# Kernel tuning notes

Hardware: AMD Instinct MI355X
Metric: run time of the kernel (lower is better)

## Reference

```python
import jax, jax.numpy as jnp
import numpy as np

B, L, D, H = 8, 4096, 512, 512  # batch, seq_len, input channels, hidden_dim
EPS = 1e-5


def setup_inputs() -> dict:
    key = jax.random.key(0)
    ks = jax.random.split(key, 6)
    sD = 1.0 / np.sqrt(D)
    sH = 1.0 / np.sqrt(H)
    return {
        "x": jax.random.normal(ks[0], (B, L, D), jnp.float32),
        "ln_gamma": jnp.ones((D,), jnp.float32),
        "ln_beta": jnp.zeros((D,), jnp.float32),
        "W_B": jax.random.normal(ks[1], (D, H), jnp.float32) * sD,
        "b_B": jnp.zeros((H,), jnp.float32),
        "W_C": jax.random.normal(ks[2], (D, H), jnp.float32) * sD,
        "b_C": jnp.zeros((H,), jnp.float32),
        "W_out": jax.random.normal(ks[3], (H, H), jnp.float32) * sH,
        "b_out": jnp.zeros((H,), jnp.float32),
        # original initializes A to zeros; use decays in (0,1) for a non-trivial scan
        "A": jax.random.uniform(ks[4], (H,), jnp.float32, 0.1, 0.95),
    }


def _scan_op(e1, e2):
    # composition of affine maps h -> a*h + b (elementwise, per channel)
    a1, b1 = e1
    a2, b2 = e2
    return a1 * a2, a2 * b1 + b2


def reference(x, ln_gamma, ln_beta, W_B, b_B, W_C, b_C, W_out, b_out, A):
    # LayerNorm over channels
    mu = jnp.mean(x, axis=-1, keepdims=True)
    var = jnp.var(x, axis=-1, keepdims=True)
    xn = (x - mu) * jax.lax.rsqrt(var + EPS) * ln_gamma + ln_beta  # [B,L,D]

    Bt = jnp.einsum("bld,dh->blh", xn, W_B) + b_B  # [B,L,H]
    Ct = jnp.einsum("bld,dh->blh", xn, W_C) + b_C  # [B,L,H]

    # linear recurrence h_t = A * h_{t-1} + B_t via associative scan over L
    a_full = jnp.broadcast_to(A, Bt.shape)
    _, h = jax.lax.associative_scan(_scan_op, (a_full, Bt), axis=1)  # [B,L,H]

    y = Ct * h  # selective readout
    return jnp.einsum("blh,ho->blo", y, W_out) + b_out  # [B,L,H]
```

## Files before the change

kernel.cpp:

```cpp
#include <hip/hip_runtime.h>
#include <hip/hip_bf16.h>
#include <stdint.h>

typedef __bf16 bf16x8 __attribute__((ext_vector_type(8)));
typedef float f32x4 __attribute__((ext_vector_type(4)));

constexpr int Bn = 8, Ln = 4096, Dn = 512, Hn = 512;
constexpr int Mrows = Bn * Ln;
constexpr int CHUNK = 64, NCHUNK = Ln / CHUNK;

__global__ __launch_bounds__(256) void prep_kernel(
    const float* __restrict__ W_B, const float* __restrict__ W_C,
    const float* __restrict__ W_out, const float* __restrict__ b_B,
    const float* __restrict__ b_C,
    __hip_bfloat16* __restrict__ WbcT, __hip_bfloat16* __restrict__ WoT,
    float* __restrict__ bbc)
{
    int id = blockIdx.x * 256 + threadIdx.x;
    {
        int n = id >> 9, k = id & 511;
        float w = (n < Hn) ? W_B[k * Hn + n] : W_C[k * Hn + (n - Hn)];
        WbcT[id] = __float2bfloat16(w);
    }
    if (id < Hn * Hn) {
        int n = id >> 9, k = id & 511;
        WoT[id] = __float2bfloat16(W_out[k * Hn + n]);
    }
    if (id < 2 * Hn) bbc[id] = (id < Hn) ? b_B[id] : b_C[id - Hn];
}

__global__ __launch_bounds__(256) void ln_kernel(
    const float* __restrict__ x, const float* __restrict__ gamma,
    const float* __restrict__ beta, __hip_bfloat16* __restrict__ xn)
{
    int row = blockIdx.x;
    const float2* xr = reinterpret_cast<const float2*>(x + (size_t)row * Dn);
    int t = threadIdx.x;
    float2 v = xr[t];
    float s = v.x + v.y;
    float s2 = v.x * v.x + v.y * v.y;
    #pragma unroll
    for (int off = 32; off; off >>= 1) {
        s  += __shfl_down(s, off);
        s2 += __shfl_down(s2, off);
    }
    __shared__ float ps[4], ps2[4];
    int wid = t >> 6, lane = t & 63;
    if (lane == 0) { ps[wid] = s; ps2[wid] = s2; }
    __syncthreads();
    float su = ps[0] + ps[1] + ps[2] + ps[3];
    float su2 = ps2[0] + ps2[1] + ps2[2] + ps2[3];
    float mu = su * (1.0f / Dn);
    float var = su2 * (1.0f / Dn) - mu * mu;
    float inv = rsqrtf(var + 1e-5f);
    int c0 = 2 * t;
    float y0 = (v.x - mu) * inv * gamma[c0]     + beta[c0];
    float y1 = (v.y - mu) * inv * gamma[c0 + 1] + beta[c0 + 1];
    __hip_bfloat162 o;
    o.x = __float2bfloat16(y0);
    o.y = __float2bfloat16(y1);
    reinterpret_cast<__hip_bfloat162*>(xn + (size_t)row * Dn)[t] = o;
}

template <int NT, bool OUT_BF16>
__global__ __launch_bounds__(512, 2) void gemm8_kernel(
    const __hip_bfloat16* __restrict__ A,
    const __hip_bfloat16* __restrict__ BT,
    const float* __restrict__ bias,
    void* __restrict__ Cout)
{
    constexpr int K = 512, NKT = K / 64, NIT = NKT / 2;
    extern __shared__ unsigned short lds[];

    int nwg = gridDim.x, bid = blockIdx.x;
    int bswz = (bid & 7) * (nwg >> 3) + (bid >> 3);
    constexpr int NBN = NT / 256;
    int bm = bswz / NBN, bnb = bswz % NBN;
    int row0 = bm * 256, col0 = bnb * 256;

    int tid = threadIdx.x;
    int w = tid >> 6, l = tid & 63;
    int rl = l & 15, qg = l >> 4, sx = l & 7, r8 = l >> 3;

    int scol = (sx ^ r8) * 8;
    const __hip_bfloat16* gA = A  + (size_t)(row0 + w * 16 + r8) * K + scol;
    const __hip_bfloat16* gB = BT + (size_t)(col0 + w * 16 + r8) * K + scol;

#define LDSA(b, h) (&lds[(b) * 32768 + (h) * 8192 + w * 1024])
#define LDSB(b, h) (&lds[(b) * 32768 + 16384 + (h) * 8192 + w * 1024])
#define GLDS(src, dst) __builtin_amdgcn_global_load_lds( \
        (const __attribute__((address_space(1))) void*)(const void*)(src), \
        (__attribute__((address_space(3))) void*)(void*)(dst), 16, 0, 0)
#define STAGE_A(b, kt, h) { \
        GLDS(gA + (size_t)((h) * 128) * K + (kt) * 64, LDSA(b, h)); \
        GLDS(gA + (size_t)((h) * 128 + 8) * K + (kt) * 64, LDSA(b, h) + 512); }
#define STAGE_B(b, kt, h) { \
        GLDS(gB + (size_t)((h) * 128) * K + (kt) * 64, LDSB(b, h)); \
        GLDS(gB + (size_t)((h) * 128 + 8) * K + (kt) * 64, LDSB(b, h) + 512); }
#define BARRIER { asm volatile("" ::: "memory"); __builtin_amdgcn_s_barrier(); \
                  asm volatile("" ::: "memory"); }
#define VMCNT(n) asm volatile("s_waitcnt vmcnt(" #n ")" ::: "memory")

    int aoff = (w >> 2) * 8192 + rl * 64;
    int boff = 16384 + ((w & 3) >> 1) * 8192 + (((w & 3) & 1) * 64 + rl) * 64;
    int s0 = (qg ^ sx) * 8;

    f32x4 acc[8][4] = {};
    bf16x8 af[4][2], bfr[4][2];

#define RD_A(mq, b) { _Pragma("unroll") for (int i2 = 0; i2 < 4; ++i2) { \
        af[i2][0] = *(const bf16x8*)&lds[(b) * 32768 + aoff + ((mq) * 4 + i2) * 1024 + s0]; \
        af[i2][1] = *(const bf16x8*)&lds[(b) * 32768 + aoff + ((mq) * 4 + i2) * 1024 + (s0 ^ 32)]; } }
#define RD_B(nh, b) { _Pragma("unroll") for (int j2 = 0; j2 < 2; ++j2) { \
        bfr[(nh) * 2 + j2][0] = *(const bf16x8*)&lds[(b) * 32768 + boff + ((nh) * 2 + j2) * 1024 + s0]; \
        bfr[(nh) * 2 + j2][1] = *(const bf16x8*)&lds[(b) * 32768 + boff + ((nh) * 2 + j2) * 1024 + (s0 ^ 32)]; } }
#define MM(mq, nq) { __builtin_amdgcn_s_setprio(1); \
        _Pragma("unroll") for (int i2 = 0; i2 < 4; ++i2) \
        _Pragma("unroll") for (int n2 = 0; n2 < 2; ++n2) \
        _Pragma("unroll") for (int kk = 0; kk < 2; ++kk) \
            acc[(mq) * 4 + i2][(nq) * 2 + n2] = __builtin_amdgcn_mfma_f32_16x16x32_bf16( \
                af[i2][kk], bfr[(nq) * 2 + n2][kk], acc[(mq) * 4 + i2][(nq) * 2 + n2], 0, 0, 0); \
        __builtin_amdgcn_s_setprio(0); }

    STAGE_B(0, 0, 0); STAGE_B(0, 0, 1); STAGE_A(0, 0, 0); STAGE_A(0, 0, 1);
    STAGE_B(1, 1, 0); STAGE_B(1, 1, 1); STAGE_A(1, 1, 0);
    VMCNT(6);
    BARRIER;

    for (int it = 0; it < NIT; ++it) {
        int ktB = 2 * it + 1, ktN = 2 * it + 2;
        bool more = (it < NIT - 1);
        RD_A(0, 0); RD_B(0, 0);
        STAGE_A(1, ktB, 1);
        BARRIER; MM(0, 0); BARRIER;
        RD_B(1, 0);
        if (more) STAGE_B(0, ktN, 0);
        BARRIER; MM(0, 1); BARRIER;
        RD_A(1, 0);
        if (more) STAGE_B(0, ktN, 1);
        BARRIER; MM(1, 1); BARRIER;
        if (more) STAGE_A(0, ktN, 0);
        BARRIER; MM(1, 0);
        if (more) { VMCNT(6); } else { VMCNT(0); }
        BARRIER;
        RD_A(0, 1); RD_B(0, 1);
        if (more) STAGE_A(0, ktN, 1);
        BARRIER; MM(0, 0); BARRIER;
        RD_B(1, 1);
        if (more) STAGE_B(1, ktN + 1, 0);
        BARRIER; MM(0, 1); BARRIER;
        RD_A(1, 1);
        if (more) STAGE_B(1, ktN + 1, 1);
        BARRIER; MM(1, 1); BARRIER;
        if (more) {
            STAGE_A(1, ktN + 1, 0);
            BARRIER; MM(1, 0); VMCNT(6); BARRIER;
        } else {
            MM(1, 0);
        }
    }

    int crow0 = row0 + (w >> 2) * 128 + qg * 4;
    int ccol0 = col0 + (w & 3) * 64 + rl;
    #pragma unroll
    for (int n = 0; n < 4; ++n) {
        float bv = bias[ccol0 + n * 16];
        #pragma unroll
        for (int i = 0; i < 8; ++i) {
            #pragma unroll
            for (int j = 0; j < 4; ++j) {
                float v = acc[i][n][j] + bv;
                size_t idx = (size_t)(crow0 + i * 16 + j) * NT + (ccol0 + n * 16);
                if (OUT_BF16)
                    ((__hip_bfloat16*)Cout)[idx] = __float2bfloat16(v);
                else
                    ((float*)Cout)[idx] = v;
            }
        }
    }
#undef LDSA
#undef LDSB
#undef GLDS
#undef STAGE_A
#undef STAGE_B
#undef BARRIER
#undef VMCNT
#undef RD_A
#undef RD_B
#undef MM
}

__global__ __launch_bounds__(256) void scan1_kernel(
    const __hip_bfloat16* __restrict__ BC, const float* __restrict__ Av,
    float* __restrict__ S)
{
    int blk = blockIdx.x;
    int hh = (blk & 1) * 256 + threadIdx.x;
    int c = (blk >> 1) & (NCHUNK - 1);
    int b = blk >> 7;
    float a = Av[hh];
    const __hip_bfloat16* p = BC + ((size_t)(b * Ln + c * CHUNK) * 1024) + hh;
    float s = 0.f;
    #pragma unroll 8
    for (int i = 0; i < CHUNK; ++i) {
        float bv = __bfloat162float(p[(size_t)i * 1024]);
        s = a * s + bv;
    }
    S[((size_t)b * NCHUNK + c) * Hn + hh] = s;
}

__global__ __launch_bounds__(256) void scan2_kernel(
    const float* __restrict__ S, const float* __restrict__ Av,
    float* __restrict__ carry)
{
    int id = blockIdx.x * 256 + threadIdx.x;
    int hh = id & (Hn - 1), b = id >> 9;
    float a = Av[hh];
    float aG = a;
    #pragma unroll
    for (int i = 0; i < 6; ++i) aG *= aG;
    float h = 0.f;
    const float* Sp = S + (size_t)b * NCHUNK * Hn + hh;
    float* cp = carry + (size_t)b * NCHUNK * Hn + hh;
    for (int c = 0; c < NCHUNK; ++c) {
        cp[(size_t)c * Hn] = h;
        h = aG * h + Sp[(size_t)c * Hn];
    }
}

__global__ __launch_bounds__(256) void scan3_kernel(
    const __hip_bfloat16* __restrict__ BC, const float* __restrict__ Av,
    const float* __restrict__ carry, __hip_bfloat16* __restrict__ Y)
{
    int blk = blockIdx.x;
    int hh = (blk & 1) * 256 + threadIdx.x;
    int c = (blk >> 1) & (NCHUNK - 1);
    int b = blk >> 7;
    float a = Av[hh];
    float h = carry[((size_t)b * NCHUNK + c) * Hn + hh];
    const __hip_bfloat16* p = BC + ((size_t)(b * Ln + c * CHUNK) * 1024) + hh;
    __hip_bfloat16* yp = Y + ((size_t)(b * Ln + c * CHUNK) * Hn) + hh;
    #pragma unroll 8
    for (int i = 0; i < CHUNK; ++i) {
        float bv = __bfloat162float(p[(size_t)i * 1024]);
        float cv = __bfloat162float(p[(size_t)i * 1024 + 512]);
        h = a * h + bv;
        yp[(size_t)i * Hn] = __float2bfloat16(cv * h);
    }
}

extern "C" void kernel_launch(void* const* d_in, const int* in_sizes, int n_in,
                              void* d_out, int out_size, void* d_ws, size_t ws_size,
                              hipStream_t stream)
{
    const float* x     = (const float*)d_in[0];
    const float* ln_g  = (const float*)d_in[1];
    const float* ln_b  = (const float*)d_in[2];
    const float* W_B   = (const float*)d_in[3];
    const float* b_B   = (const float*)d_in[4];
    const float* W_C   = (const float*)d_in[5];
    const float* b_C   = (const float*)d_in[6];
    const float* W_out = (const float*)d_in[7];
    const float* b_out = (const float*)d_in[8];
    const float* Avec  = (const float*)d_in[9];

    char* ws = (char*)d_ws;
    __hip_bfloat16* WbcT = (__hip_bfloat16*)(ws);
    __hip_bfloat16* WoT  = (__hip_bfloat16*)(ws + (1u << 20));
    float*          bbc  = (float*)(ws + (1u << 20) + (1u << 19));
    __hip_bfloat16* XN   = (__hip_bfloat16*)(ws + (2u << 20));
    __hip_bfloat16* BC   = (__hip_bfloat16*)(ws + (34u << 20));
    float*          Sbuf = (float*)(ws + (98u << 20));
    float*          Cbuf = (float*)(ws + (99u << 20));
    __hip_bfloat16* Y    = (__hip_bfloat16*)(ws + (100u << 20));

    hipFuncSetAttribute((const void*)gemm8_kernel<1024, true>,
                        hipFuncAttributeMaxDynamicSharedMemorySize, 131072);
    hipFuncSetAttribute((const void*)gemm8_kernel<512, false>,
                        hipFuncAttributeMaxDynamicSharedMemorySize, 131072);

    prep_kernel<<<2048, 256, 0, stream>>>(W_B, W_C, W_out, b_B, b_C, WbcT, WoT, bbc);
    ln_kernel<<<Mrows, 256, 0, stream>>>(x, ln_g, ln_b, XN);
    gemm8_kernel<1024, true><<<(Mrows / 256) * (1024 / 256), 512, 131072, stream>>>(
        XN, WbcT, bbc, BC);
    scan1_kernel<<<Bn * NCHUNK * 2, 256, 0, stream>>>(BC, Avec, Sbuf);
    scan2_kernel<<<(Bn * Hn) / 256, 256, 0, stream>>>(Sbuf, Avec, Cbuf);
    scan3_kernel<<<Bn * NCHUNK * 2, 256, 0, stream>>>(BC, Avec, Cbuf, Y);
    gemm8_kernel<512, false><<<(Mrows / 256) * (512 / 256), 512, 131072, stream>>>(
        Y, WoT, b_out, d_out);
}
```

Before: 134.5 us.

## Shrink GEMM tiles to 128x128 with 4-wave workgroups

Replaces the 256x256-tile, 8-wave GEMM with a 128x128-tile, 4-wave version that uses 64KB of LDS. The staging schedule, LDS swizzle addressing and wave-to-subtile mapping are rewritten to fit the smaller tile. The aim is more workgroups for better CU load balance and occupancy, since the second GEMM previously launched only 256 blocks. The trade-off is lower data reuse per tile, which means more global/L2 traffic and more LDS reads per MFMA.

After: 136.6 us. No clear change (+1.5%).

```diff
diff --git a/kernel.cpp b/kernel.cpp
--- a/kernel.cpp
+++ b/kernel.cpp
@@ -63,110 +63,109 @@
 }
 
 template <int NT, bool OUT_BF16>
-__global__ __launch_bounds__(512, 2) void gemm8_kernel(
+__global__ __launch_bounds__(256, 2) void gemm4_kernel(
     const __hip_bfloat16* __restrict__ A,
     const __hip_bfloat16* __restrict__ BT,
     const float* __restrict__ bias,
     void* __restrict__ Cout)
 {
-    constexpr int K = 512, NKT = K / 64, NIT = NKT / 2;
+    constexpr int K = 512, NIT = 4;
     extern __shared__ unsigned short lds[];
 
     int nwg = gridDim.x, bid = blockIdx.x;
     int bswz = (bid & 7) * (nwg >> 3) + (bid >> 3);
-    constexpr int NBN = NT / 256;
+    constexpr int NBN = NT / 128;
     int bm = bswz / NBN, bnb = bswz % NBN;
-    int row0 = bm * 256, col0 = bnb * 256;
+    int row0 = bm * 128, col0 = bnb * 128;
 
     int tid = threadIdx.x;
     int w = tid >> 6, l = tid & 63;
-    int rl = l & 15, qg = l >> 4, sx = l & 7, r8 = l >> 3;
-
-    int scol = (sx ^ r8) * 8;
-    const __hip_bfloat16* gA = A  + (size_t)(row0 + w * 16 + r8) * K + scol;
-    const __hip_bfloat16* gB = BT + (size_t)(col0 + w * 16 + r8) * K + scol;
-
-#define LDSA(b, h) (&lds[(b) * 32768 + (h) * 8192 + w * 1024])
-#define LDSB(b, h) (&lds[(b) * 32768 + 16384 + (h) * 8192 + w * 1024])
+    int rl = l & 15, qg = l >> 4;
+
+    int scol = ((l & 7) ^ (l >> 3)) * 8;
+    const __hip_bfloat16* gA = A  + (size_t)(row0 + w * 16 + (l >> 3)) * K + scol;
+    const __hip_bfloat16* gB = BT + (size_t)(col0 + w * 16 + (l >> 3)) * K + scol;
+
 #define GLDS(src, dst) __builtin_amdgcn_global_load_lds( \
         (const __attribute__((address_space(1))) void*)(const void*)(src), \
         (__attribute__((address_space(3))) void*)(void*)(dst), 16, 0, 0)
-#define STAGE_A(b, kt, h) { \
-        GLDS(gA + (size_t)((h) * 128) * K + (kt) * 64, LDSA(b, h)); \
-        GLDS(gA + (size_t)((h) * 128 + 8) * K + (kt) * 64, LDSA(b, h) + 512); }
-#define STAGE_B(b, kt, h) { \
-        GLDS(gB + (size_t)((h) * 128) * K + (kt) * 64, LDSB(b, h)); \
-        GLDS(gB + (size_t)((h) * 128 + 8) * K + (kt) * 64, LDSB(b, h) + 512); }
+#define STA(b, kt, h, sub) GLDS(gA + (size_t)((h) * 64 + (sub) * 8) * K + (kt) * 64, \
+        &lds[(b) * 16384 + (h) * 4096 + w * 1024 + (sub) * 512])
+#define STB(b, kt, h, sub) GLDS(gB + (size_t)((h) * 64 + (sub) * 8) * K + (kt) * 64, \
+        &lds[(b) * 16384 + 8192 + (h) * 4096 + w * 1024 + (sub) * 512])
+#define STAGE_AU(b, kt, h) { STA(b, kt, h, 0); STA(b, kt, h, 1); }
+#define STAGE_BU(b, kt, h) { STB(b, kt, h, 0); STB(b, kt, h, 1); }
 #define BARRIER { asm volatile("" ::: "memory"); __builtin_amdgcn_s_barrier(); \
                   asm volatile("" ::: "memory"); }
 #define VMCNT(n) asm volatile("s_waitcnt vmcnt(" #n ")" ::: "memory")
 
-    int aoff = (w >> 2) * 8192 + rl * 64;
-    int boff = 16384 + ((w & 3) >> 1) * 8192 + (((w & 3) & 1) * 64 + rl) * 64;
-    int s0 = (qg ^ sx) * 8;
-
-    f32x4 acc[8][4] = {};
-    bf16x8 af[4][2], bfr[4][2];
-
-#define RD_A(mq, b) { _Pragma("unroll") for (int i2 = 0; i2 < 4; ++i2) { \
-        af[i2][0] = *(const bf16x8*)&lds[(b) * 32768 + aoff + ((mq) * 4 + i2) * 1024 + s0]; \
-        af[i2][1] = *(const bf16x8*)&lds[(b) * 32768 + aoff + ((mq) * 4 + i2) * 1024 + (s0 ^ 32)]; } }
-#define RD_B(nh, b) { _Pragma("unroll") for (int j2 = 0; j2 < 2; ++j2) { \
-        bfr[(nh) * 2 + j2][0] = *(const bf16x8*)&lds[(b) * 32768 + boff + ((nh) * 2 + j2) * 1024 + s0]; \
-        bfr[(nh) * 2 + j2][1] = *(const bf16x8*)&lds[(b) * 32768 + boff + ((nh) * 2 + j2) * 1024 + (s0 ^ 32)]; } }
+    int aoff = ((w >> 1) * 64 + rl) * 64;
+    int boff = 8192 + ((w & 1) * 64 + rl) * 64;
+    int s0k0 = (qg ^ (rl & 7)) * 8;
+    int s0k1 = ((4 + qg) ^ (rl & 7)) * 8;
+
+    f32x4 acc[4][4] = {};
+    bf16x8 af[2][2], bfr[4][2];
+
+#define RD_A(mq, b) { _Pragma("unroll") for (int i2 = 0; i2 < 2; ++i2) { \
+        af[i2][0] = *(const bf16x8*)&lds[(b) * 16384 + aoff + ((mq) * 32 + i2 * 16) * 64 + s0k0]; \
+        af[i2][1] = *(const bf16x8*)&lds[(b) * 16384 + aoff + ((mq) * 32 + i2 * 16) * 64 + s0k1]; } }
+#define RD_B(nq, b) { _Pragma("unroll") for (int j2 = 0; j2 < 2; ++j2) { \
+        bfr[(nq) * 2 + j2][0] = *(const bf16x8*)&lds[(b) * 16384 + boff + ((nq) * 32 + j2 * 16) * 64 + s0k0]; \
+        bfr[(nq) * 2 + j2][1] = *(const bf16x8*)&lds[(b) * 16384 + boff + ((nq) * 32 + j2 * 16) * 64 + s0k1]; } }
 #define MM(mq, nq) { __builtin_amdgcn_s_setprio(1); \
-        _Pragma("unroll") for (int i2 = 0; i2 < 4; ++i2) \
-        _Pragma("unroll") for (int n2 = 0; n2 < 2; ++n2) \
+        _Pragma("unroll") for (int i2 = 0; i2 < 2; ++i2) \
+        _Pragma("unroll") for (int j2 = 0; j2 < 2; ++j2) \
         _Pragma("unroll") for (int kk = 0; kk < 2; ++kk) \
-            acc[(mq) * 4 + i2][(nq) * 2 + n2] = __builtin_amdgcn_mfma_f32_16x16x32_bf16( \
-                af[i2][kk], bfr[(nq) * 2 + n2][kk], acc[(mq) * 4 + i2][(nq) * 2 + n2], 0, 0, 0); \
+            acc[(mq) * 2 + i2][(nq) * 2 + j2] = __builtin_amdgcn_mfma_f32_16x16x32_bf16( \
+                af[i2][kk], bfr[(nq) * 2 + j2][kk], acc[(mq) * 2 + i2][(nq) * 2 + j2], 0, 0, 0); \
         __builtin_amdgcn_s_setprio(0); }
 
-    STAGE_B(0, 0, 0); STAGE_B(0, 0, 1); STAGE_A(0, 0, 0); STAGE_A(0, 0, 1);
-    STAGE_B(1, 1, 0); STAGE_B(1, 1, 1); STAGE_A(1, 1, 0);
-    VMCNT(6);
+    STAGE_BU(0, 0, 0); STAGE_BU(0, 0, 1); STAGE_AU(0, 0, 0); STAGE_AU(0, 0, 1);
+    STAGE_BU(1, 1, 0); STAGE_BU(1, 1, 1);
+    VMCNT(4);
     BARRIER;
 
     for (int it = 0; it < NIT; ++it) {
-        int ktB = 2 * it + 1, ktN = 2 * it + 2;
+        int e = 2 * it;
         bool more = (it < NIT - 1);
         RD_A(0, 0); RD_B(0, 0);
-        STAGE_A(1, ktB, 1);
+        STAGE_AU(1, e + 1, 0);
         BARRIER; MM(0, 0); BARRIER;
         RD_B(1, 0);
-        if (more) STAGE_B(0, ktN, 0);
+        STAGE_AU(1, e + 1, 1);
         BARRIER; MM(0, 1); BARRIER;
         RD_A(1, 0);
-        if (more) STAGE_B(0, ktN, 1);
+        if (more) STAGE_BU(0, e + 2, 0);
         BARRIER; MM(1, 1); BARRIER;
-        if (more) STAGE_A(0, ktN, 0);
+        if (more) STAGE_BU(0, e + 2, 1);
         BARRIER; MM(1, 0);
-        if (more) { VMCNT(6); } else { VMCNT(0); }
+        if (more) { VMCNT(4); } else { VMCNT(0); }
         BARRIER;
         RD_A(0, 1); RD_B(0, 1);
-        if (more) STAGE_A(0, ktN, 1);
+        if (more) STAGE_AU(0, e + 2, 0);
         BARRIER; MM(0, 0); BARRIER;
         RD_B(1, 1);
-        if (more) STAGE_B(1, ktN + 1, 0);
+        if (more) STAGE_AU(0, e + 2, 1);
         BARRIER; MM(0, 1); BARRIER;
         RD_A(1, 1);
-        if (more) STAGE_B(1, ktN + 1, 1);
+        if (more) STAGE_BU(1, e + 3, 0);
         BARRIER; MM(1, 1); BARRIER;
         if (more) {
-            STAGE_A(1, ktN + 1, 0);
-            BARRIER; MM(1, 0); VMCNT(6); BARRIER;
+            STAGE_BU(1, e + 3, 1);
+            BARRIER; MM(1, 0); VMCNT(4); BARRIER;
         } else {
-            MM(1, 0);
+            BARRIER; MM(1, 0);
         }
     }
 
-    int crow0 = row0 + (w >> 2) * 128 + qg * 4;
-    int ccol0 = col0 + (w & 3) * 64 + rl;
+    int crow0 = row0 + (w >> 1) * 64 + qg * 4;
+    int ccol0 = col0 + (w & 1) * 64 + rl;
     #pragma unroll
     for (int n = 0; n < 4; ++n) {
         float bv = bias[ccol0 + n * 16];
         #pragma unroll
-        for (int i = 0; i < 8; ++i) {
+        for (int i = 0; i < 4; ++i) {
             #pragma unroll
             for (int j = 0; j < 4; ++j) {
                 float v = acc[i][n][j] + bv;
@@ -178,11 +177,11 @@
             }
         }
     }
-#undef LDSA
-#undef LDSB
 #undef GLDS
-#undef STAGE_A
-#undef STAGE_B
+#undef STA
+#undef STB
+#undef STAGE_AU
+#undef STAGE_BU
 #undef BARRIER
 #undef VMCNT
 #undef RD_A
@@ -274,18 +273,18 @@
     float*          Cbuf = (float*)(ws + (99u << 20));
     __hip_bfloat16* Y    = (__hip_bfloat16*)(ws + (100u << 20));
 
-    hipFuncSetAttribute((const void*)gemm8_kernel<1024, true>,
-                        hipFuncAttributeMaxDynamicSharedMemorySize, 131072);
-    hipFuncSetAttribute((const void*)gemm8_kernel<512, false>,
-                        hipFuncAttributeMaxDynamicSharedMemorySize, 131072);
+    hipFuncSetAttribute((const void*)gemm4_kernel<1024, true>,
+                        hipFuncAttributeMaxDynamicSharedMemorySize, 65536);
+    hipFuncSetAttribute((const void*)gemm4_kernel<512, false>,
+                        hipFuncAttributeMaxDynamicSharedMemorySize, 65536);
 
     prep_kernel<<<2048, 256, 0, stream>>>(W_B, W_C, W_out, b_B, b_C, WbcT, WoT, bbc);
     ln_kernel<<<Mrows, 256, 0, stream>>>(x, ln_g, ln_b, XN);
-    gemm8_kernel<1024, true><<<(Mrows / 256) * (1024 / 256), 512, 131072, stream>>>(
+    gemm4_kernel<1024, true><<<(Mrows / 128) * (1024 / 128), 256, 65536, stream>>>(
         XN, WbcT, bbc, BC);
     scan1_kernel<<<Bn * NCHUNK * 2, 256, 0, stream>>>(BC, Avec, Sbuf);
     scan2_kernel<<<(Bn * Hn) / 256, 256, 0, stream>>>(Sbuf, Avec, Cbuf);
     scan3_kernel<<<Bn * NCHUNK * 2, 256, 0, stream>>>(BC, Avec, Cbuf, Y);
-    gemm8_kernel<512, false><<<(Mrows / 256) * (512 / 256), 512, 131072, stream>>>(
+    gemm4_kernel<512, false><<<(Mrows / 128) * (512 / 128), 256, 65536, stream>>>(
         Y, WoT, b_out, d_out);
 }
```
